# Kernel optimization log

Measured on AMD Instinct MI355X. Metric: run time of the kernel, lower is better.

## Reference

```python
import jax, jax.numpy as jnp
import numpy as np

N_NODES = 10000
N_EDGES = 160000
N_TYPES = 128          # rows in SymbolicEmbeddingsVQ table
N_SYMBOLS = 64
PATTERN_LEN = 8
SYMBOL_DIM = 16
HIDDEN = PATTERN_LEN * SYMBOL_DIM  # mode='concat' -> 128
NUM_RADIAL = 6


def setup_inputs() -> dict:
    key = jax.random.key(0)
    ks = jax.random.split(key, 10)
    x = jax.random.randint(ks[0], (N_NODES,), 0, N_TYPES)
    rbf = jax.random.normal(ks[1], (N_EDGES, NUM_RADIAL), dtype=jnp.float32)
    i = jax.random.randint(ks[2], (N_EDGES,), 0, N_NODES)
    j = jax.random.randint(ks[3], (N_EDGES,), 0, N_NODES)
    # VQ symbolic embedding params: each of 128 types is a pattern of
    # PATTERN_LEN symbol ids; symbols are vectors from a codebook.
    code_idx = jax.random.randint(ks[4], (N_TYPES, PATTERN_LEN), 0, N_SYMBOLS)
    codebook = jax.random.normal(ks[5], (N_SYMBOLS, SYMBOL_DIM), dtype=jnp.float32)
    # Linear layers (PyTorch Linear default uniform init approximated by scaled normals)
    W_rbf = jax.random.normal(ks[6], (NUM_RADIAL, HIDDEN), dtype=jnp.float32) / np.sqrt(NUM_RADIAL)
    b_rbf = jnp.zeros((HIDDEN,), dtype=jnp.float32)
    W = jax.random.normal(ks[7], (3 * HIDDEN, HIDDEN), dtype=jnp.float32) / np.sqrt(3 * HIDDEN)
    b = jnp.zeros((HIDDEN,), dtype=jnp.float32)
    return {"x": x, "rbf": rbf, "i": i, "j": j, "code_idx": code_idx,
            "codebook": codebook, "W_rbf": W_rbf, "b_rbf": b_rbf, "W": W, "b": b}


def reference(x, rbf, i, j, code_idx, codebook, W_rbf, b_rbf, W, b):
    act = jax.nn.silu
    # Symbolic VQ embedding, mode='concat': table[t] = concat of PATTERN_LEN codebook vectors
    table = codebook[code_idx].reshape(N_TYPES, HIDDEN)   # [128, hidden]
    h = table[x]                                          # [N_nodes, hidden]
    r = act(rbf @ W_rbf + b_rbf)                          # [E, hidden]
    feat = jnp.concatenate([h[i], h[j], r], axis=-1)      # [E, 3*hidden]
    return act(feat @ W + b)                              # [E, hidden]
```

## Files before the change

kernel.cpp:

```cpp
#include <hip/hip_runtime.h>
#include <hip/hip_bf16.h>
#include <stdint.h>

typedef __attribute__((ext_vector_type(8))) short bf16x8;
typedef __attribute__((ext_vector_type(4))) float f32x4;
typedef __attribute__((ext_vector_type(4))) unsigned short u16x4;

__device__ __forceinline__ float silu_f(float x) {
    return x * __builtin_amdgcn_rcpf(1.0f + __expf(-x));
}

__device__ __forceinline__ unsigned short f2bf(float x) {
    union { float f; unsigned int u; } v; v.f = x;
    unsigned int r = v.u + 0x7fffu + ((v.u >> 16) & 1u);
    return (unsigned short)(r >> 16);
}
__device__ __forceinline__ float bf2f(unsigned short u) {
    union { unsigned int u; float f; } v; v.u = ((unsigned int)u) << 16;
    return v.f;
}

__device__ __forceinline__ void async16(void* l, const void* g) {
    auto lds3 = (__attribute__((address_space(3))) unsigned int*)(uintptr_t)l;
    auto g1   = (const __attribute__((address_space(1))) unsigned int*)(uintptr_t)g;
    __builtin_amdgcn_global_load_lds(g1, lds3, 16, 0, 0);
}

__global__ void prep_P(const int* __restrict__ code_idx,
                       const float* __restrict__ codebook,
                       const float* __restrict__ W,
                       const float* __restrict__ b,
                       unsigned short* __restrict__ P1,
                       unsigned short* __restrict__ P2,
                       unsigned short* __restrict__ Wt3)
{
    __shared__ float trow[128];
    const int t = blockIdx.x, tid = threadIdx.x;
    if (tid < 128) {
        int sym = code_idx[t * 8 + (tid >> 4)];
        trow[tid] = codebook[sym * 16 + (tid & 15)];
    } else {
        int k = tid - 128;
        Wt3[t * 128 + k] = f2bf(W[(256 + k) * 128 + t]);
    }
    __syncthreads();
    const int which = tid >> 7, o = tid & 127;
    const float* Wb = W + which * 16384;
    float acc = which ? 0.0f : b[o];
#pragma unroll 8
    for (int k = 0; k < 128; ++k)
        acc += trow[k] * Wb[k * 128 + o];
    (which ? P2 : P1)[t * 128 + o] = f2bf(acc);
}

__global__ __launch_bounds__(256, 3) void fused_main(
    const int* __restrict__ x,
    const float* __restrict__ rbf,
    const int* __restrict__ ei,
    const int* __restrict__ ej,
    const float* __restrict__ W_rbf,
    const float* __restrict__ b_rbf,
    const unsigned short* __restrict__ P1,
    const unsigned short* __restrict__ P2,
    const unsigned short* __restrict__ Wt3,
    float* __restrict__ out)
{
    __shared__ __align__(16) unsigned char lA[16384];
    __shared__ __align__(16) unsigned char lR[1536];

    const int tid  = threadIdx.x;
    const int lane = tid & 63;
    const int w    = tid >> 6;
    const int e0   = blockIdx.x * 64;

    const int quad = lane >> 4, l15 = lane & 15;
    const int wm = (w >> 1) * 32, wn = (w & 1) * 64;

    if (w == 0)
        async16(lR, (const unsigned char*)rbf + (size_t)e0 * 24 + lane * 16);
    else if (w == 1 && lane < 32)
        async16(lR + 1024, (const unsigned char*)rbf + (size_t)e0 * 24 + 1024 + lane * 16);

    int ti[2], tj[2];
#pragma unroll
    for (int mi = 0; mi < 2; ++mi) {
        int e = e0 + wm + mi * 16 + l15;
        ti[mi] = x[ei[e]];
        tj[mi] = x[ej[e]];
    }

    const int j16 = tid & 15, gg = tid >> 4, cb = j16 * 8;
    float wr[6][8], br[8];
#pragma unroll
    for (int q = 0; q < 6; ++q) {
        const float4* p = (const float4*)(W_rbf + q * 128 + cb);
        float4 a = p[0], c = p[1];
        wr[q][0]=a.x; wr[q][1]=a.y; wr[q][2]=a.z; wr[q][3]=a.w;
        wr[q][4]=c.x; wr[q][5]=c.y; wr[q][6]=c.z; wr[q][7]=c.w;
    }
    {
        const float4* p = (const float4*)(b_rbf + cb);
        float4 a = p[0], c = p[1];
        br[0]=a.x; br[1]=a.y; br[2]=a.z; br[3]=a.w;
        br[4]=c.x; br[5]=c.y; br[6]=c.z; br[7]=c.w;
    }

    __syncthreads();

#pragma unroll
    for (int i = 0; i < 4; ++i) {
        int m = gg * 4 + i;
        const float* rr_ = (const float*)(lR + m * 24);
        float f0 = rr_[0], f1 = rr_[1], f2 = rr_[2],
              f3 = rr_[3], f4 = rr_[4], f5 = rr_[5];
        bf16x8 pk;
#pragma unroll
        for (int c = 0; c < 8; ++c) {
            float a = br[c] + f0*wr[0][c] + f1*wr[1][c] + f2*wr[2][c]
                            + f3*wr[3][c] + f4*wr[4][c] + f5*wr[5][c];
            pk[c] = (short)f2bf(silu_f(a));
        }
        int p = j16 ^ (m & 7);
        *(bf16x8*)(lA + m * 256 + p * 16) = pk;
    }

    bf16x8 Bf[4][4];
#pragma unroll
    for (int ni = 0; ni < 4; ++ni) {
        const unsigned short* brow = Wt3 + (wn + ni * 16 + l15) * 128 + quad * 8;
#pragma unroll
        for (int ks = 0; ks < 4; ++ks)
            Bf[ni][ks] = *(const bf16x8*)(brow + ks * 32);
    }

    u16x4 q1[2][4], q2[2][4];
#pragma unroll
    for (int mi = 0; mi < 2; ++mi) {
        const unsigned short* p1r = P1 + ti[mi] * 128;
        const unsigned short* p2r = P2 + tj[mi] * 128;
#pragma unroll
        for (int ni = 0; ni < 4; ++ni) {
            int o = wn + ni * 16 + quad * 4;
            q1[mi][ni] = *(const u16x4*)(p1r + o);
            q2[mi][ni] = *(const u16x4*)(p2r + o);
        }
    }

    __syncthreads();

    f32x4 acc[2][4] = {};
    const int l7 = l15 & 7;
#pragma unroll
    for (int ks = 0; ks < 4; ++ks) {
        const int j = ks * 4 + quad;
        const int p = j ^ l7;
        bf16x8 af[2];
#pragma unroll
        for (int mi = 0; mi < 2; ++mi)
            af[mi] = *(const bf16x8*)(lA + (wm + mi * 16 + l15) * 256 + p * 16);
#pragma unroll
        for (int mi = 0; mi < 2; ++mi)
#pragma unroll
            for (int ni = 0; ni < 4; ++ni)
                acc[mi][ni] = __builtin_amdgcn_mfma_f32_16x16x32_bf16(
                    Bf[ni][ks], af[mi], acc[mi][ni], 0, 0, 0);
    }

#pragma unroll
    for (int mi = 0; mi < 2; ++mi) {
        size_t e = (size_t)(e0 + wm + mi * 16 + l15);
        float* orow = out + e * 128 + wn;
#pragma unroll
        for (int ni = 0; ni < 4; ++ni) {
            f32x4 v;
#pragma unroll
            for (int r = 0; r < 4; ++r)
                v[r] = silu_f(acc[mi][ni][r]
                              + bf2f(q1[mi][ni][r]) + bf2f(q2[mi][ni][r]));
            *(f32x4*)(orow + ni * 16 + quad * 4) = v;
        }
    }
}

extern "C" void kernel_launch(void* const* d_in, const int* in_sizes, int n_in,
                              void* d_out, int out_size, void* d_ws, size_t ws_size,
                              hipStream_t stream) {
    const int*   x        = (const int*)d_in[0];
    const float* rbf      = (const float*)d_in[1];
    const int*   ei       = (const int*)d_in[2];
    const int*   ej       = (const int*)d_in[3];
    const int*   code_idx = (const int*)d_in[4];
    const float* codebook = (const float*)d_in[5];
    const float* W_rbf    = (const float*)d_in[6];
    const float* b_rbf    = (const float*)d_in[7];
    const float* W        = (const float*)d_in[8];
    const float* b        = (const float*)d_in[9];
    float* out = (float*)d_out;

    const int nE = in_sizes[2];

    if (ws_size < 98304) return;
    unsigned short* P1  = (unsigned short*)d_ws;
    unsigned short* P2  = P1 + 16384;
    unsigned short* Wt3 = P2 + 16384;

    prep_P<<<128, 256, 0, stream>>>(code_idx, codebook, W, b, P1, P2, Wt3);
    fused_main<<<nE / 64, 256, 0, stream>>>(x, rbf, ei, ej, W_rbf, b_rbf,
                                            P1, P2, Wt3, out);
}
```

Measured before the change: 156.5 us.

## Use 512-thread blocks and stage Wt3 in swizzled LDS for B fragments

Each block now runs 8 waves instead of 4, so every wave handles 16 edges rather than 32 and the per-thread gather and rbf work is halved. The 32 KB Wt3 weight tile is copied into LDS with async global-to-LDS loads and an XOR swizzle, and B fragments are read from LDS instead of global memory. The goal is more latency hiding and less per-thread register pressure. In exchange, LDS per block grows to about 50 KB, which may cap how many blocks fit on a CU, and every block still copies the whole weight tile.

```diff
diff --git a/kernel.cpp b/kernel.cpp
--- a/kernel.cpp
+++ b/kernel.cpp
@@ -53,7 +53,7 @@
     (which ? P2 : P1)[t * 128 + o] = f2bf(acc);
 }
 
-__global__ __launch_bounds__(256, 3) void fused_main(
+__global__ __launch_bounds__(512, 6) void fused_main(
     const int* __restrict__ x,
     const float* __restrict__ rbf,
     const int* __restrict__ ei,
@@ -65,6 +65,7 @@
     const unsigned short* __restrict__ Wt3,
     float* __restrict__ out)
 {
+    __shared__ __align__(16) unsigned char lB[32768];
     __shared__ __align__(16) unsigned char lA[16384];
     __shared__ __align__(16) unsigned char lR[1536];
 
@@ -73,20 +74,30 @@
     const int w    = tid >> 6;
     const int e0   = blockIdx.x * 64;
 
-    const int quad = lane >> 4, l15 = lane & 15;
-    const int wm = (w >> 1) * 32, wn = (w & 1) * 64;
-
+    const int quad = lane >> 4, l15 = lane & 15, l7 = l15 & 7;
+    const int wm = (w >> 1) * 16;
+    const int wn = (w & 1) * 64;
+
+    {
+        const int ri = lane >> 4, ch = lane & 15;
+#pragma unroll
+        for (int rr = 0; rr < 4; ++rr) {
+            int g = w * 4 + rr;
+            int o = g * 4 + ri;
+            int jc = ch ^ (o & 7);
+            async16(lB + g * 1024, Wt3 + o * 128 + jc * 8);
+        }
+    }
     if (w == 0)
         async16(lR, (const unsigned char*)rbf + (size_t)e0 * 24 + lane * 16);
     else if (w == 1 && lane < 32)
         async16(lR + 1024, (const unsigned char*)rbf + (size_t)e0 * 24 + 1024 + lane * 16);
 
-    int ti[2], tj[2];
-#pragma unroll
-    for (int mi = 0; mi < 2; ++mi) {
-        int e = e0 + wm + mi * 16 + l15;
-        ti[mi] = x[ei[e]];
-        tj[mi] = x[ej[e]];
+    int ti, tj;
+    {
+        int e = e0 + wm + l15;
+        ti = x[ei[e]];
+        tj = x[ej[e]];
     }
 
     const int j16 = tid & 15, gg = tid >> 4, cb = j16 * 8;
@@ -108,8 +119,8 @@
     __syncthreads();
 
 #pragma unroll
-    for (int i = 0; i < 4; ++i) {
-        int m = gg * 4 + i;
+    for (int i = 0; i < 2; ++i) {
+        int m = gg * 2 + i;
         const float* rr_ = (const float*)(lR + m * 24);
         float f0 = rr_[0], f1 = rr_[1], f2 = rr_[2],
               f3 = rr_[3], f4 = rr_[4], f5 = rr_[5];
@@ -124,59 +135,49 @@
         *(bf16x8*)(lA + m * 256 + p * 16) = pk;
     }
 
+    u16x4 q1[4], q2[4];
+#pragma unroll
+    for (int ni = 0; ni < 4; ++ni) {
+        int o = wn + ni * 16 + quad * 4;
+        q1[ni] = *(const u16x4*)(P1 + ti * 128 + o);
+        q2[ni] = *(const u16x4*)(P2 + tj * 128 + o);
+    }
+
+    __syncthreads();
+
     bf16x8 Bf[4][4];
 #pragma unroll
     for (int ni = 0; ni < 4; ++ni) {
-        const unsigned short* brow = Wt3 + (wn + ni * 16 + l15) * 128 + quad * 8;
+        const unsigned char* brow = lB + (wn + ni * 16 + l15) * 256;
 #pragma unroll
         for (int ks = 0; ks < 4; ++ks)
-            Bf[ni][ks] = *(const bf16x8*)(brow + ks * 32);
-    }
-
-    u16x4 q1[2][4], q2[2][4];
-#pragma unroll
-    for (int mi = 0; mi < 2; ++mi) {
-        const unsigned short* p1r = P1 + ti[mi] * 128;
-        const unsigned short* p2r = P2 + tj[mi] * 128;
-#pragma unroll
-        for (int ni = 0; ni < 4; ++ni) {
-            int o = wn + ni * 16 + quad * 4;
-            q1[mi][ni] = *(const u16x4*)(p1r + o);
-            q2[mi][ni] = *(const u16x4*)(p2r + o);
-        }
-    }
-
-    __syncthreads();
-
-    f32x4 acc[2][4] = {};
-    const int l7 = l15 & 7;
-#pragma unroll
-    for (int ks = 0; ks < 4; ++ks) {
-        const int j = ks * 4 + quad;
-        const int p = j ^ l7;
-        bf16x8 af[2];
-#pragma unroll
-        for (int mi = 0; mi < 2; ++mi)
-            af[mi] = *(const bf16x8*)(lA + (wm + mi * 16 + l15) * 256 + p * 16);
-#pragma unroll
-        for (int mi = 0; mi < 2; ++mi)
-#pragma unroll
-            for (int ni = 0; ni < 4; ++ni)
-                acc[mi][ni] = __builtin_amdgcn_mfma_f32_16x16x32_bf16(
-                    Bf[ni][ks], af[mi], acc[mi][ni], 0, 0, 0);
-    }
-
-#pragma unroll
-    for (int mi = 0; mi < 2; ++mi) {
-        size_t e = (size_t)(e0 + wm + mi * 16 + l15);
+            Bf[ni][ks] = *(const bf16x8*)(brow + (((ks * 4 + quad) ^ l7) * 16));
+    }
+    bf16x8 af[4];
+    {
+        const unsigned char* arow = lA + (wm + l15) * 256;
+#pragma unroll
+        for (int ks = 0; ks < 4; ++ks)
+            af[ks] = *(const bf16x8*)(arow + (((ks * 4 + quad) ^ l7) * 16));
+    }
+
+    f32x4 acc[4] = {};
+#pragma unroll
+    for (int ks = 0; ks < 4; ++ks)
+#pragma unroll
+        for (int ni = 0; ni < 4; ++ni)
+            acc[ni] = __builtin_amdgcn_mfma_f32_16x16x32_bf16(
+                Bf[ni][ks], af[ks], acc[ni], 0, 0, 0);
+
+    {
+        size_t e = (size_t)(e0 + wm + l15);
         float* orow = out + e * 128 + wn;
 #pragma unroll
         for (int ni = 0; ni < 4; ++ni) {
             f32x4 v;
 #pragma unroll
             for (int r = 0; r < 4; ++r)
-                v[r] = silu_f(acc[mi][ni][r]
-                              + bf2f(q1[mi][ni][r]) + bf2f(q2[mi][ni][r]));
+                v[r] = silu_f(acc[ni][r] + bf2f(q1[ni][r]) + bf2f(q2[ni][r]));
             *(f32x4*)(orow + ni * 16 + quad * 4) = v;
         }
     }
@@ -205,6 +206,6 @@
     unsigned short* Wt3 = P2 + 16384;
 
     prep_P<<<128, 256, 0, stream>>>(code_idx, codebook, W, b, P1, P2, Wt3);
-    fused_main<<<nE / 64, 256, 0, stream>>>(x, rbf, ei, ej, W_rbf, b_rbf,
+    fused_main<<<nE / 64, 512, 0, stream>>>(x, rbf, ei, ej, W_rbf, b_rbf,
                                             P1, P2, Wt3, out);
 }
```

Result: faster. 152.8 us (-2.4%).
